# Performance work log

Measured on AMD Instinct MI355X. Metric: run time of the kernel, lower is better.

Reference implementation:

```python
import jax, jax.numpy as jnp
import numpy as np

NUM_CLASSES = 80
SCORE_THR = 0.2
NMS_THR = 0.3
MAX_PER_IMAGE = 100
TOPK_PER_CLASS = 100  # cap on pre-NMS candidates per (image, class); >= max_per_image
ANCHOR_MASK = [[6, 7, 8], [3, 4, 5], [0, 1, 2]]
COCO_ANCHORS = np.array([[10, 13], [16, 30], [33, 23], [30, 61], [62, 45],
                         [59, 119], [116, 90], [156, 198], [373, 326]], dtype=np.float32)


def yolo_head(feats, layer_anchors, num_classes, input_shape):
    # feats: [B, 3*(5+C), gh, gw]
    B = feats.shape[0]
    gh, gw = feats.shape[2], feats.shape[3]
    na = layer_anchors.shape[0]
    f = feats.reshape(B, na, num_classes + 5, gh, gw).transpose(0, 3, 4, 1, 2)  # [B,gh,gw,3,5+C]
    gy, gx = jnp.meshgrid(jnp.arange(gh), jnp.arange(gw), indexing='ij')
    grid = jnp.stack([gx, gy], axis=-1).astype(f.dtype)[None, :, :, None, :]  # [1,gh,gw,1,2]
    # literal translation: divide by tensor([gh, gw]) (square grids in practice)
    box_xy = (jax.nn.sigmoid(f[..., :2]) + grid) / jnp.array([gh, gw], f.dtype)
    box_wh = jnp.exp(f[..., 2:4]) * layer_anchors[None, None, None, :, :] / input_shape[None, None, None, None, :]
    conf = jax.nn.sigmoid(f[..., 4:5])
    probs = jax.nn.sigmoid(f[..., 5:])
    return box_xy, box_wh, conf, probs


def yolo_correct_boxes(box_xy, box_wh, input_shape, image_shape):
    box_yx = box_xy[..., ::-1]
    box_hw = box_wh[..., ::-1]
    new_shape = jnp.round(image_shape * jnp.min(input_shape / image_shape))
    offset = (input_shape - new_shape) / 2.0 / input_shape
    scale = input_shape / new_shape
    box_yx = (box_yx - offset) * scale
    box_hw = box_hw * scale
    mins = box_yx - box_hw / 2.0
    maxes = box_yx + box_hw / 2.0
    boxes = jnp.concatenate([mins, maxes], axis=-1)  # (ymin, xmin, ymax, xmax)
    return boxes * jnp.concatenate([image_shape, image_shape])


def decode_layer(feats, layer_anchors, input_shape, image_shape):
    box_xy, box_wh, conf, probs = yolo_head(feats, layer_anchors, NUM_CLASSES, input_shape)
    boxes = yolo_correct_boxes(box_xy, box_wh, input_shape, image_shape)  # [B,gh,gw,3,4]
    B = feats.shape[0]
    return boxes.reshape(B, -1, 4), (conf * probs).reshape(B, -1, NUM_CLASSES)


def pairwise_iou(b):
    # b: [K,4] (y1,x1,y2,x2)
    y1, x1, y2, x2 = b[:, 0], b[:, 1], b[:, 2], b[:, 3]
    area = jnp.maximum(y2 - y1, 0) * jnp.maximum(x2 - x1, 0)
    iy1 = jnp.maximum(y1[:, None], y1[None, :])
    ix1 = jnp.maximum(x1[:, None], x1[None, :])
    iy2 = jnp.minimum(y2[:, None], y2[None, :])
    ix2 = jnp.minimum(x2[:, None], x2[None, :])
    inter = jnp.maximum(iy2 - iy1, 0) * jnp.maximum(ix2 - ix1, 0)
    return inter / (area[:, None] + area[None, :] - inter + 1e-9)


def greedy_nms(boxes, valid):
    # boxes [K,4] sorted by descending score; valid [K] bool. Returns keep mask [K].
    K = boxes.shape[0]
    iou = jax.lax.stop_gradient(pairwise_iou(boxes))
    idx = jnp.arange(K)
    def body(i, sup):
        keep_i = valid[i] & (~sup[i])
        return sup | (keep_i & (iou[i] > NMS_THR) & (idx > i))
    sup = jax.lax.fori_loop(0, K, body, jnp.zeros((K,), bool))
    return valid & (~sup)


def setup_inputs() -> dict:
    key = jax.random.key(0)
    k0, k1, k2 = jax.random.split(key, 3)
    B, F = 16, 3 * (5 + NUM_CLASSES)
    feat0 = jax.random.normal(k0, (B, F, 19, 19), jnp.float32)
    feat1 = jax.random.normal(k1, (B, F, 38, 38), jnp.float32)
    feat2 = jax.random.normal(k2, (B, F, 76, 76), jnp.float32)
    anchors = jnp.asarray(COCO_ANCHORS)
    image_shape = jnp.array([480.0, 640.0], jnp.float32)
    return {"feat0": feat0, "feat1": feat1, "feat2": feat2,
            "anchors": anchors, "image_shape": image_shape}


def reference(feat0, feat1, feat2, anchors, image_shape):
    input_shape = jnp.array([feat0.shape[2] * 32, feat0.shape[3] * 32], jnp.float32)
    feats = [feat0, feat1, feat2]
    boxes_l, scores_l = [], []
    for l in range(3):
        b, s = decode_layer(feats[l], anchors[np.array(ANCHOR_MASK[l])], input_shape, image_shape)
        boxes_l.append(b)
        scores_l.append(s)
    boxes = jnp.concatenate(boxes_l, axis=1)    # [B,N,4]
    scores = jnp.concatenate(scores_l, axis=1)  # [B,N,C]
    B = scores.shape[0]
    sc = scores.transpose(0, 2, 1)              # [B,C,N]
    top_s, top_i = jax.lax.top_k(sc, TOPK_PER_CLASS)              # [B,C,K]
    top_b = jnp.take_along_axis(boxes[:, None, :, :], top_i[..., None], axis=2)  # [B,C,K,4]
    valid = top_s >= SCORE_THR
    keep = jax.vmap(jax.vmap(greedy_nms))(top_b, valid)           # [B,C,K]
    cand = jnp.where(keep, top_s, -1.0)
    flat_s = cand.reshape(B, -1)                 # [B, C*K]
    flat_b = top_b.reshape(B, -1, 4)
    sel_s, sel_i = jax.lax.top_k(flat_s, MAX_PER_IMAGE)           # [B,100]
    sel_b = jnp.take_along_axis(flat_b, sel_i[..., None], axis=1)  # [B,100,4]
    sel_c = (sel_i // TOPK_PER_CLASS).astype(jnp.float32)
    # dets: (ymin, xmin, ymax, xmax, score, class); score == -1 marks padding
    return jnp.concatenate([sel_b, sel_s[..., None], sel_c[..., None]], axis=-1)
```

## Files before the change

kernel.cpp:

```cpp
#include <hip/hip_runtime.h>
#include <hip/hip_bf16.h>


#define NTOT   22743
#define NCLS   80
#define TOPK   100
#define KPAD   22752
#define NVEC   2842
#define Q_L1   17328
#define Q_L0   21660
#define SCORE_THR 0.2f
#define NMS_THR   0.3f

__device__ __forceinline__ float sig_exact(float x) {
    return 1.0f / (1.0f + expf(-x));
}
__device__ __forceinline__ float sig_fast(float x) {
    return __builtin_amdgcn_rcpf(1.0f + __expf(-x));
}

__global__ __launch_bounds__(256) void k_decode(
    const float* __restrict__ f0, const float* __restrict__ f1,
    const float* __restrict__ f2, const float* __restrict__ anchors,
    const float* __restrict__ imshape, float4* __restrict__ boxes,
    float* __restrict__ conf_q, int total) {
    int gid = blockIdx.x * 256 + threadIdx.x;
    if (gid >= total) return;
    int b = gid / NTOT; int p = gid - b * NTOT;

    const float* f; int ghw, gw, l, off, a, s;
    if (p < 1083)      { f=f0; off=0;    ghw=361;  gw=19; l=0; int r=p;      a=r/361;  s=r-a*361;  }
    else if (p < 5415) { f=f1; off=1083; ghw=1444; gw=38; l=1; int r=p-1083; a=r/1444; s=r-a*1444; }
    else               { f=f2; off=5415; ghw=5776; gw=76; l=2; int r=p-5415; a=r/5776; s=r-a*5776; }
    int y = s / gw, x = s - y * gw;

    const float* q = f + ((size_t)(b * 255 + a * 85) * ghw + s);
    float tx = q[0], ty = q[ghw], tw = q[2*ghw], th = q[3*ghw], tc = q[4*ghw];

    int arow = (2 - l) * 3 + a;
    float aw = anchors[arow * 2], ah = anchors[arow * 2 + 1];
    float imh = imshape[0], imw = imshape[1];
    float gf = (float)gw;

    float bxx = (sig_exact(tx) + (float)x) / gf;
    float bxy = (sig_exact(ty) + (float)y) / gf;
    float bw  = expf(tw) * aw / 608.0f;
    float bh  = expf(th) * ah / 608.0f;

    float r  = fminf(608.0f / imh, 608.0f / imw);
    float nh = rintf(imh * r), nw = rintf(imw * r);
    float offy = (608.0f - nh) / 2.0f / 608.0f;
    float offx = (608.0f - nw) / 2.0f / 608.0f;
    float scy = 608.0f / nh, scx = 608.0f / nw;

    float cy = (bxy - offy) * scy;
    float cx = (bxx - offx) * scx;
    float hh = bh * scy, ww = bw * scx;

    int n = off + 3 * s + a;
    boxes[(size_t)b * NTOT + n] =
        make_float4((cy - hh / 2.0f) * imh, (cx - ww / 2.0f) * imw,
                    (cy + hh / 2.0f) * imh, (cx + ww / 2.0f) * imw);
    int qi = (l == 2) ? (a * 5776 + s)
           : (l == 1) ? (Q_L1 + a * 1444 + s)
                      : (Q_L0 + a * 361 + s);
    conf_q[(size_t)b * KPAD + qi] = sig_exact(tc);
}

#define SEG_A  346560
#define SEG_AB 433200
#define SEG_T  519840
__global__ __launch_bounds__(256) void k_score(
    const float* __restrict__ f0, const float* __restrict__ f1,
    const float* __restrict__ f2, const float* __restrict__ conf_q,
    unsigned short* __restrict__ keybuf, int total) {
    int gid = blockIdx.x * 256 + threadIdx.x;
    if (gid >= total) return;
    const int b = gid / SEG_T;
    const int w = gid - b * SEG_T;

    if (w < SEG_AB) {
        const float* f; int a, c, s, qbase, ghw;
        if (w < SEG_A) {
            a = w / 115520; int r = w - a * 115520;
            c = r / 1444;   s = (r - c * 1444) * 4;
            f = f2; ghw = 5776; qbase = a * 5776;
        } else {
            int t = w - SEG_A;
            a = t / 28880;  int r = t - a * 28880;
            c = r / 361;    s = (r - c * 361) * 4;
            f = f1; ghw = 1444; qbase = Q_L1 + a * 1444;
        }
        const float4 lg = *(const float4*)(f + ((size_t)(b * 255 + a * 85 + 5 + c) * ghw + s));
        const float4 cf = *(const float4*)(conf_q + (size_t)b * KPAD + qbase + s);
        ushort4 k;
        k.x = (unsigned short)(__float_as_uint(cf.x * sig_fast(lg.x)) >> 16);
        k.y = (unsigned short)(__float_as_uint(cf.y * sig_fast(lg.y)) >> 16);
        k.z = (unsigned short)(__float_as_uint(cf.z * sig_fast(lg.z)) >> 16);
        k.w = (unsigned short)(__float_as_uint(cf.w * sig_fast(lg.w)) >> 16);
        *(ushort4*)(keybuf + ((size_t)(b * NCLS + c)) * KPAD + qbase + s) = k;
    } else {
        int t = w - SEG_AB;
        int a = t / 28880;  int r = t - a * 28880;
        int c = r / 361;    int s = r - c * 361;
        int qi = Q_L0 + a * 361 + s;
        float lg = f0[((size_t)(b * 255 + a * 85 + 5 + c) * 361 + s)];
        float cf = conf_q[(size_t)b * KPAD + qi];
        keybuf[((size_t)(b * NCLS + c)) * KPAD + qi] =
            (unsigned short)(__float_as_uint(cf * sig_fast(lg)) >> 16);
    }
}

__device__ void find_pivot(unsigned* hist, int H, unsigned target,
                           unsigned* suf, unsigned* sh_p, unsigned* sh_above) {
    const int tid = threadIdx.x;
    const int per = H >> 8;
    if (tid < 256) {
        unsigned acc = 0;
        for (int u = 0; u < per; ++u) acc += hist[tid * per + u];
        suf[tid] = acc;
    }
    __syncthreads();
    for (int off = 1; off < 256; off <<= 1) {
        unsigned v = 0;
        if (tid < 256) v = (tid + off < 256) ? suf[tid + off] : 0u;
        __syncthreads();
        if (tid < 256) suf[tid] += v;
        __syncthreads();
    }
    if (tid < 256) {
        unsigned mysuf = suf[tid];
        unsigned nxt = (tid == 255) ? 0u : suf[tid + 1];
        if (mysuf >= target && nxt < target) {
            unsigned above = nxt;
            for (int h = tid * per + per - 1; h >= tid * per; --h) {
                unsigned c2 = above + hist[h];
                if (c2 >= target) { *sh_p = (unsigned)h; *sh_above = above; break; }
                above = c2;
            }
        }
    }
    __syncthreads();
}

__device__ __forceinline__ void collect_cand(
    int b, int c, int q, const float* __restrict__ f0,
    const float* __restrict__ f1, const float* __restrict__ f2,
    const float* __restrict__ conf_q, unsigned long long* buf,
    unsigned* sh_cnt) {
    int a, s, nbase, ghw;
    const float* f;
    if (q < Q_L1)      { a = q / 5776;  s = q - a * 5776;  f = f2; ghw = 5776; nbase = 5415; }
    else if (q < Q_L0) { int r = q - Q_L1; a = r / 1444; s = r - a * 1444; f = f1; ghw = 1444; nbase = 1083; }
    else               { int r = q - Q_L0; a = r / 361;  s = r - a * 361;  f = f0; ghw = 361;  nbase = 0;    }
    float t  = f[((size_t)(b * 255 + a * 85 + 5 + c)) * ghw + s];
    float cf = conf_q[(size_t)b * KPAD + q];
    float sce = cf * sig_exact(t);
    int n = nbase + 3 * s + a;
    unsigned slot = atomicAdd(sh_cnt, 1u);
    if (slot < 512)
        buf[slot] = (((unsigned long long)__float_as_uint(sce)) << 32)
                    | (unsigned)(~n);
}

__global__ __launch_bounds__(512, 8) void k_topk(
    const float* __restrict__ f0, const float* __restrict__ f1,
    const float* __restrict__ f2, const float* __restrict__ conf_q,
    const unsigned short* __restrict__ keybuf,
    const float4* __restrict__ boxes, float* __restrict__ top_s,
    float4* __restrict__ top_b) {
    __shared__ unsigned int histp[4096];
    __shared__ unsigned long long buf[512];
    __shared__ unsigned int wsum[4];
    __shared__ unsigned int sh_p, sh_cnt;

    const int tid = threadIdx.x;
    const int row = blockIdx.x;
    const int b = row / NCLS, c = row - b * NCLS;
    const unsigned short* kr = keybuf + (size_t)row * KPAD;
    const uint4* kv = (const uint4*)kr;

    for (int i = tid; i < 4096; i += 512) histp[i] = 0;
    if (tid == 0) sh_cnt = 0;
    __syncthreads();

    uint4 v[6];
    bool  val[6];
    #pragma unroll
    for (int k = 0; k < 6; ++k) {
        int g = tid + k * 512;
        val[k] = (g < NVEC);
        v[k] = val[k] ? kv[g] : make_uint4(0, 0, 0, 0);
    }
    const bool hastail = (tid < NTOT - NVEC * 8);
    unsigned tailk = hastail ? (unsigned)kr[NVEC * 8 + tid] : 0u;

    #pragma unroll
    for (int k = 0; k < 6; ++k) if (val[k]) {
        unsigned ks[8] = { v[k].x & 0xFFFFu, v[k].x >> 16, v[k].y & 0xFFFFu, v[k].y >> 16,
                           v[k].z & 0xFFFFu, v[k].z >> 16, v[k].w & 0xFFFFu, v[k].w >> 16 };
        #pragma unroll
        for (int j = 0; j < 8; ++j)
            atomicAdd(&histp[ks[j] >> 2], 1u << (((ks[j] >> 1) & 1u) * 16));
    }
    if (hastail) atomicAdd(&histp[tailk >> 2], 1u << (((tailk >> 1) & 1u) * 16));
    __syncthreads();

    {
        const int lane = tid & 63;
        unsigned own = 0;
        if (tid < 256) {
            #pragma unroll
            for (int u = 0; u < 16; ++u) {
                unsigned w = histp[tid * 16 + u];
                own += (w & 0xFFFFu) + (w >> 16);
            }
        }
        unsigned acc = own;
        #pragma unroll
        for (int d = 1; d < 64; d <<= 1) {
            unsigned vv = __shfl_down(acc, d, 64);
            if (lane + d < 64) acc += vv;
        }
        if (tid < 256 && lane == 0) wsum[tid >> 6] = acc;
        __syncthreads();
        if (tid < 256) {
            unsigned tail = 0;
            for (int w2 = (tid >> 6) + 1; w2 < 4; ++w2) tail += wsum[w2];
            unsigned suft = acc + tail;
            unsigned nxt  = suft - own;
            if (suft >= TOPK && nxt < TOPK) {
                unsigned above = nxt;
                for (int bb = 31; bb >= 0; --bb) {
                    unsigned w = histp[tid * 16 + (bb >> 1)];
                    unsigned cnt = (bb & 1) ? (w >> 16) : (w & 0xFFFFu);
                    if (above + cnt >= TOPK) { sh_p = (unsigned)(tid * 32 + bb); break; }
                    above += cnt;
                }
            }
        }
        __syncthreads();
    }
    const unsigned kthr = sh_p > 0 ? ((sh_p - 1) << 1) : 0u;

    #pragma unroll
    for (int k = 0; k < 6; ++k) if (val[k]) {
        unsigned ks[8] = { v[k].x & 0xFFFFu, v[k].x >> 16, v[k].y & 0xFFFFu, v[k].y >> 16,
                           v[k].z & 0xFFFFu, v[k].z >> 16, v[k].w & 0xFFFFu, v[k].w >> 16 };
        #pragma unroll
        for (int j = 0; j < 8; ++j)
            if (ks[j] >= kthr)
                collect_cand(b, c, (tid + k * 512) * 8 + j, f0, f1, f2, conf_q, buf, &sh_cnt);
    }
    if (hastail && tailk >= kthr)
        collect_cand(b, c, NVEC * 8 + tid, f0, f1, f2, conf_q, buf, &sh_cnt);
    __syncthreads();

    const int M = (int)min(sh_cnt, 512u);
    if (tid < M) {
        unsigned long long mykey = buf[tid];
        int rank = 0;
        for (int j = 0; j < M; ++j) rank += (buf[j] > mykey);
        if (rank < TOPK) {
            int n = (int)(~(unsigned)mykey);
            top_s[(size_t)row * TOPK + rank] = __uint_as_float((unsigned)(mykey >> 32));
            top_b[(size_t)row * TOPK + rank] = boxes[(size_t)b * NTOT + n];
        }
    }
}

__global__ __launch_bounds__(256) void k_nms(
    const float* __restrict__ top_s, const float4* __restrict__ top_b,
    float* __restrict__ cand) {
    const int lane = threadIdx.x & 63;
    const int row  = blockIdx.x * 4 + (threadIdx.x >> 6);
    const float4* bb = top_b + (size_t)row * TOPK;
    const float*  ss = top_s + (size_t)row * TOPK;

    const int j0 = lane, j1 = lane + 64;
    const bool v1 = (j1 < TOPK);
    float4 B0 = bb[j0];
    float  s0 = ss[j0];
    float4 B1 = v1 ? bb[j1] : make_float4(0.f, 0.f, 0.f, 0.f);
    float  s1 = v1 ? ss[j1] : -1.0f;
    float ar0 = fmaxf(B0.z - B0.x, 0.f) * fmaxf(B0.w - B0.y, 0.f);
    float ar1 = fmaxf(B1.z - B1.x, 0.f) * fmaxf(B1.w - B1.y, 0.f);
    int sup0 = 0, sup1 = 0;

    for (int i = 0; i < TOPK; ++i) {
        const int src = i & 63;
        const bool hi = (i >= 64);
        float yi1 = __shfl(hi ? B1.x : B0.x, src, 64);
        float xi1 = __shfl(hi ? B1.y : B0.y, src, 64);
        float yi2 = __shfl(hi ? B1.z : B0.z, src, 64);
        float xi2 = __shfl(hi ? B1.w : B0.w, src, 64);
        float si  = __shfl(hi ? s1   : s0,   src, 64);
        int  supi = __shfl(hi ? sup1 : sup0, src, 64);
        bool keep_i = (si >= SCORE_THR) && (supi == 0);
        if (keep_i) {
            float ari = fmaxf(yi2 - yi1, 0.f) * fmaxf(xi2 - xi1, 0.f);
            if (j0 > i) {
                float ty1 = fmaxf(yi1, B0.x), tx1 = fmaxf(xi1, B0.y);
                float ty2 = fminf(yi2, B0.z), tx2 = fminf(xi2, B0.w);
                float inter = fmaxf(ty2 - ty1, 0.f) * fmaxf(tx2 - tx1, 0.f);
                float iou = inter / (ari + ar0 - inter + 1e-9f);
                if (iou > NMS_THR) sup0 = 1;
            }
            if (v1 && j1 > i) {
                float ty1 = fmaxf(yi1, B1.x), tx1 = fmaxf(xi1, B1.y);
                float ty2 = fminf(yi2, B1.z), tx2 = fminf(xi2, B1.w);
                float inter = fmaxf(ty2 - ty1, 0.f) * fmaxf(tx2 - tx1, 0.f);
                float iou = inter / (ari + ar1 - inter + 1e-9f);
                if (iou > NMS_THR) sup1 = 1;
            }
        }
    }
    cand[(size_t)row * TOPK + j0] = (s0 >= SCORE_THR && sup0 == 0) ? s0 : -1.0f;
    if (v1)
        cand[(size_t)row * TOPK + j1] = (s1 >= SCORE_THR && sup1 == 0) ? s1 : -1.0f;
}

__global__ __launch_bounds__(256) void k_final(
    const float* __restrict__ cand, const float4* __restrict__ top_b,
    float* __restrict__ out) {
    __shared__ float cs[8000];
    __shared__ unsigned int hist[4096];
    __shared__ unsigned long long buf[512];
    __shared__ unsigned int suf[256];
    __shared__ unsigned int sh_kp, sh_p1, sh_above1, sh_p2, sh_above2, sh_cnt;

    const int tid = threadIdx.x, b = blockIdx.x;
    if (tid == 0) { sh_kp = 0; sh_cnt = 0; }
    for (int i = tid; i < 4096; i += 256) hist[i] = 0;
    __syncthreads();

    unsigned lk = 0;
    for (int i = tid; i < 8000; i += 256) {
        float v = cand[b * 8000 + i];
        cs[i] = v;
        if (v > -0.5f) lk++;
    }
    atomicAdd(&sh_kp, lk);
    __syncthreads();
    unsigned Kp = sh_kp;

    if (Kp >= TOPK) {
        for (int i = tid; i < 8000; i += 256)
            if (cs[i] > -0.5f) atomicAdd(&hist[__float_as_uint(cs[i]) >> 19], 1u);
        __syncthreads();
        find_pivot(hist, 2048, TOPK, suf, &sh_p1, &sh_above1);
        unsigned p1 = sh_p1, above1 = sh_above1;
        for (int i = tid; i < 4096; i += 256) hist[i] = 0;
        __syncthreads();
        for (int i = tid; i < 8000; i += 256) {
            float v = cs[i];
            if (v > -0.5f) {
                unsigned bits = __float_as_uint(v);
                if ((bits >> 19) == p1) atomicAdd(&hist[(bits >> 7) & 0xFFFu], 1u);
            }
        }
        __syncthreads();
        find_pivot(hist, 4096, TOPK - above1, suf, &sh_p2, &sh_above2);
        unsigned p2 = sh_p2;
        for (int i = tid; i < 8000; i += 256) {
            float v = cs[i];
            if (v > -0.5f) {
                unsigned bits = __float_as_uint(v);
                unsigned b1 = bits >> 19;
                if (b1 > p1 || (b1 == p1 && ((bits >> 7) & 0xFFFu) >= p2)) {
                    unsigned slot = atomicAdd(&sh_cnt, 1u);
                    if (slot < 512)
                        buf[slot] = (((unsigned long long)bits) << 32) | (unsigned)(~i);
                }
            }
        }
    } else {
        for (int i = tid; i < 8000; i += 256) {
            float v = cs[i];
            if (v > -0.5f) {
                unsigned slot = atomicAdd(&sh_cnt, 1u);
                buf[slot] = (((unsigned long long)__float_as_uint(v)) << 32) | (unsigned)(~i);
            }
        }
        __syncthreads();
        if (tid == 0) {
            unsigned need = TOPK - Kp, got = 0;
            for (int i = 0; i < 8000 && got < need; ++i)
                if (cs[i] <= -0.5f) { buf[Kp + got] = (unsigned)(~i); got++; }
        }
    }
    __syncthreads();

    const int M2 = (Kp >= TOPK) ? (int)min(sh_cnt, 512u) : (int)TOPK;
    for (int i = tid; i < M2; i += 256) {
        unsigned long long key = buf[i];
        int rank = 0;
        for (int j = 0; j < M2; ++j) rank += (buf[j] > key);
        if (rank < TOPK) {
            int fi = (int)(~(unsigned)key);
            int c = fi / TOPK; int kk = fi - c * TOPK;
            float4 bb = top_b[((size_t)b * NCLS + c) * TOPK + kk];
            int base = (b * TOPK + rank) * 6;
            out[base + 0] = bb.x; out[base + 1] = bb.y;
            out[base + 2] = bb.z; out[base + 3] = bb.w;
            out[base + 4] = cs[fi]; out[base + 5] = (float)c;
        }
    }
}

extern "C" void kernel_launch(void* const* d_in, const int* in_sizes, int n_in,
                              void* d_out, int out_size, void* d_ws, size_t ws_size,
                              hipStream_t stream) {
    (void)n_in; (void)out_size; (void)ws_size;
    const float* f0      = (const float*)d_in[0];
    const float* f1      = (const float*)d_in[1];
    const float* f2      = (const float*)d_in[2];
    const float* anchors = (const float*)d_in[3];
    const float* imshape = (const float*)d_in[4];
    const int B = in_sizes[0] / (255 * 19 * 19);

    char* ws = (char*)d_ws;
    size_t o = 0;
    unsigned short* keybuf = (unsigned short*)(ws + o);
    o += (size_t)B * NCLS * KPAD * sizeof(unsigned short);
    float4* boxes  = (float4*)(ws + o); o += (size_t)B * NTOT * sizeof(float4);
    float*  conf_q = (float*)(ws + o);  o += (size_t)B * KPAD * sizeof(float);
    float*  top_s  = (float*)(ws + o);  o += (size_t)B * NCLS * TOPK * sizeof(float);
    float4* top_b  = (float4*)(ws + o); o += (size_t)B * NCLS * TOPK * sizeof(float4);
    float*  cand   = (float*)(ws + o);  o += (size_t)B * NCLS * TOPK * sizeof(float);
    float*  out    = (float*)d_out;

    const int total = B * NTOT;
    k_decode<<<(total + 255) / 256, 256, 0, stream>>>(f0, f1, f2, anchors, imshape,
                                                      boxes, conf_q, total);
    const int stotal = B * SEG_T;
    k_score<<<(stotal + 255) / 256, 256, 0, stream>>>(f0, f1, f2, conf_q,
                                                      keybuf, stotal);
    k_topk<<<B * NCLS, 512, 0, stream>>>(f0, f1, f2, conf_q, keybuf, boxes,
                                         top_s, top_b);
    k_nms<<<(B * NCLS) / 4, 256, 0, stream>>>(top_s, top_b, cand);
    k_final<<<B, 256, 0, stream>>>(cand, top_b, out);
}
```

Measured before the change: 266.7 us.

## Fuse class-score computation into top-k kernel, drop keybuf round trip

Removes the separate k_score kernel that wrote 16-bit score keys for every (image, class, anchor) to a global key buffer. k_topk now reads the class logits and confidences directly, computes the keys in registers, and builds its histogram from them, keeping the keys in registers for the candidate-collection pass. This eliminates one kernel launch and the write and reread of the key buffer. In exchange k_topk carries more registers per thread and more arithmetic, and its input reads are spread across three feature maps.

```diff
diff --git a/kernel.cpp b/kernel.cpp
--- a/kernel.cpp
+++ b/kernel.cpp
@@ -6,9 +6,9 @@
 #define NCLS   80
 #define TOPK   100
 #define KPAD   22752
-#define NVEC   2842
 #define Q_L1   17328
 #define Q_L0   21660
+#define NVQ    5415
 #define SCORE_THR 0.2f
 #define NMS_THR   0.3f
 
@@ -65,82 +65,6 @@
            : (l == 1) ? (Q_L1 + a * 1444 + s)
                       : (Q_L0 + a * 361 + s);
     conf_q[(size_t)b * KPAD + qi] = sig_exact(tc);
-}
-
-#define SEG_A  346560
-#define SEG_AB 433200
-#define SEG_T  519840
-__global__ __launch_bounds__(256) void k_score(
-    const float* __restrict__ f0, const float* __restrict__ f1,
-    const float* __restrict__ f2, const float* __restrict__ conf_q,
-    unsigned short* __restrict__ keybuf, int total) {
-    int gid = blockIdx.x * 256 + threadIdx.x;
-    if (gid >= total) return;
-    const int b = gid / SEG_T;
-    const int w = gid - b * SEG_T;
-
-    if (w < SEG_AB) {
-        const float* f; int a, c, s, qbase, ghw;
-        if (w < SEG_A) {
-            a = w / 115520; int r = w - a * 115520;
-            c = r / 1444;   s = (r - c * 1444) * 4;
-            f = f2; ghw = 5776; qbase = a * 5776;
-        } else {
-            int t = w - SEG_A;
-            a = t / 28880;  int r = t - a * 28880;
-            c = r / 361;    s = (r - c * 361) * 4;
-            f = f1; ghw = 1444; qbase = Q_L1 + a * 1444;
-        }
-        const float4 lg = *(const float4*)(f + ((size_t)(b * 255 + a * 85 + 5 + c) * ghw + s));
-        const float4 cf = *(const float4*)(conf_q + (size_t)b * KPAD + qbase + s);
-        ushort4 k;
-        k.x = (unsigned short)(__float_as_uint(cf.x * sig_fast(lg.x)) >> 16);
-        k.y = (unsigned short)(__float_as_uint(cf.y * sig_fast(lg.y)) >> 16);
-        k.z = (unsigned short)(__float_as_uint(cf.z * sig_fast(lg.z)) >> 16);
-        k.w = (unsigned short)(__float_as_uint(cf.w * sig_fast(lg.w)) >> 16);
-        *(ushort4*)(keybuf + ((size_t)(b * NCLS + c)) * KPAD + qbase + s) = k;
-    } else {
-        int t = w - SEG_AB;
-        int a = t / 28880;  int r = t - a * 28880;
-        int c = r / 361;    int s = r - c * 361;
-        int qi = Q_L0 + a * 361 + s;
-        float lg = f0[((size_t)(b * 255 + a * 85 + 5 + c) * 361 + s)];
-        float cf = conf_q[(size_t)b * KPAD + qi];
-        keybuf[((size_t)(b * NCLS + c)) * KPAD + qi] =
-            (unsigned short)(__float_as_uint(cf * sig_fast(lg)) >> 16);
-    }
-}
-
-__device__ void find_pivot(unsigned* hist, int H, unsigned target,
-                           unsigned* suf, unsigned* sh_p, unsigned* sh_above) {
-    const int tid = threadIdx.x;
-    const int per = H >> 8;
-    if (tid < 256) {
-        unsigned acc = 0;
-        for (int u = 0; u < per; ++u) acc += hist[tid * per + u];
-        suf[tid] = acc;
-    }
-    __syncthreads();
-    for (int off = 1; off < 256; off <<= 1) {
-        unsigned v = 0;
-        if (tid < 256) v = (tid + off < 256) ? suf[tid + off] : 0u;
-        __syncthreads();
-        if (tid < 256) suf[tid] += v;
-        __syncthreads();
-    }
-    if (tid < 256) {
-        unsigned mysuf = suf[tid];
-        unsigned nxt = (tid == 255) ? 0u : suf[tid + 1];
-        if (mysuf >= target && nxt < target) {
-            unsigned above = nxt;
-            for (int h = tid * per + per - 1; h >= tid * per; --h) {
-                unsigned c2 = above + hist[h];
-                if (c2 >= target) { *sh_p = (unsigned)h; *sh_above = above; break; }
-                above = c2;
-            }
-        }
-    }
-    __syncthreads();
 }
 
 __device__ __forceinline__ void collect_cand(
@@ -166,7 +90,6 @@
 __global__ __launch_bounds__(512, 8) void k_topk(
     const float* __restrict__ f0, const float* __restrict__ f1,
     const float* __restrict__ f2, const float* __restrict__ conf_q,
-    const unsigned short* __restrict__ keybuf,
     const float4* __restrict__ boxes, float* __restrict__ top_s,
     float4* __restrict__ top_b) {
     __shared__ unsigned int histp[4096];
@@ -177,33 +100,53 @@
     const int tid = threadIdx.x;
     const int row = blockIdx.x;
     const int b = row / NCLS, c = row - b * NCLS;
-    const unsigned short* kr = keybuf + (size_t)row * KPAD;
-    const uint4* kv = (const uint4*)kr;
+    const float* cfrow = conf_q + (size_t)b * KPAD;
 
     for (int i = tid; i < 4096; i += 512) histp[i] = 0;
     if (tid == 0) sh_cnt = 0;
     __syncthreads();
 
-    uint4 v[6];
-    bool  val[6];
+    uint2 kreg[11];
     #pragma unroll
-    for (int k = 0; k < 6; ++k) {
-        int g = tid + k * 512;
-        val[k] = (g < NVEC);
-        v[k] = val[k] ? kv[g] : make_uint4(0, 0, 0, 0);
-    }
-    const bool hastail = (tid < NTOT - NVEC * 8);
-    unsigned tailk = hastail ? (unsigned)kr[NVEC * 8 + tid] : 0u;
-
+    for (int k = 0; k < 11; ++k) {
+        const int g = tid + k * 512;
+        const bool valid = (k < 10) || (g < NVQ);
+        kreg[k] = make_uint2(0u, 0u);
+        if (valid) {
+            const int q = g * 4;
+            const float* lp; int s;
+            if (q < Q_L1) { int a = q / 5776; s = q - a * 5776;
+                lp = f2 + (size_t)(b * 255 + a * 85 + 5 + c) * 5776; }
+            else          { int r = q - Q_L1; int a = r / 1444; s = r - a * 1444;
+                lp = f1 + (size_t)(b * 255 + a * 85 + 5 + c) * 1444; }
+            const float4 lg = *(const float4*)(lp + s);
+            const float4 cf = *(const float4*)(cfrow + q);
+            unsigned kx = __float_as_uint(cf.x * sig_fast(lg.x)) >> 16;
+            unsigned ky = __float_as_uint(cf.y * sig_fast(lg.y)) >> 16;
+            unsigned kz = __float_as_uint(cf.z * sig_fast(lg.z)) >> 16;
+            unsigned kw = __float_as_uint(cf.w * sig_fast(lg.w)) >> 16;
+            kreg[k] = make_uint2(kx | (ky << 16), kz | (kw << 16));
+            atomicAdd(&histp[kx >> 2], 1u << (((kx >> 1) & 1u) * 16));
+            atomicAdd(&histp[ky >> 2], 1u << (((ky >> 1) & 1u) * 16));
+            atomicAdd(&histp[kz >> 2], 1u << (((kz >> 1) & 1u) * 16));
+            atomicAdd(&histp[kw >> 2], 1u << (((kw >> 1) & 1u) * 16));
+        }
+    }
+    unsigned k0[3];
     #pragma unroll
-    for (int k = 0; k < 6; ++k) if (val[k]) {
-        unsigned ks[8] = { v[k].x & 0xFFFFu, v[k].x >> 16, v[k].y & 0xFFFFu, v[k].y >> 16,
-                           v[k].z & 0xFFFFu, v[k].z >> 16, v[k].w & 0xFFFFu, v[k].w >> 16 };
-        #pragma unroll
-        for (int j = 0; j < 8; ++j)
-            atomicAdd(&histp[ks[j] >> 2], 1u << (((ks[j] >> 1) & 1u) * 16));
-    }
-    if (hastail) atomicAdd(&histp[tailk >> 2], 1u << (((tailk >> 1) & 1u) * 16));
+    for (int it = 0; it < 3; ++it) {
+        const int idx = tid + it * 512;
+        const bool valid = (idx < NTOT - Q_L0);
+        k0[it] = 0u;
+        if (valid) {
+            const int a = idx / 361, s = idx - a * 361;
+            float lg = f0[(size_t)(b * 255 + a * 85 + 5 + c) * 361 + s];
+            float cf = cfrow[Q_L0 + idx];
+            unsigned kk = __float_as_uint(cf * sig_fast(lg)) >> 16;
+            k0[it] = kk;
+            atomicAdd(&histp[kk >> 2], 1u << (((kk >> 1) & 1u) * 16));
+        }
+    }
     __syncthreads();
 
     {
@@ -244,16 +187,24 @@
     const unsigned kthr = sh_p > 0 ? ((sh_p - 1) << 1) : 0u;
 
     #pragma unroll
-    for (int k = 0; k < 6; ++k) if (val[k]) {
-        unsigned ks[8] = { v[k].x & 0xFFFFu, v[k].x >> 16, v[k].y & 0xFFFFu, v[k].y >> 16,
-                           v[k].z & 0xFFFFu, v[k].z >> 16, v[k].w & 0xFFFFu, v[k].w >> 16 };
-        #pragma unroll
-        for (int j = 0; j < 8; ++j)
-            if (ks[j] >= kthr)
-                collect_cand(b, c, (tid + k * 512) * 8 + j, f0, f1, f2, conf_q, buf, &sh_cnt);
-    }
-    if (hastail && tailk >= kthr)
-        collect_cand(b, c, NVEC * 8 + tid, f0, f1, f2, conf_q, buf, &sh_cnt);
+    for (int k = 0; k < 11; ++k) {
+        const int g = tid + k * 512;
+        if ((k < 10) || (g < NVQ)) {
+            const int q = g * 4;
+            unsigned ks[4] = { kreg[k].x & 0xFFFFu, kreg[k].x >> 16,
+                               kreg[k].y & 0xFFFFu, kreg[k].y >> 16 };
+            #pragma unroll
+            for (int j = 0; j < 4; ++j)
+                if (ks[j] >= kthr)
+                    collect_cand(b, c, q + j, f0, f1, f2, conf_q, buf, &sh_cnt);
+        }
+    }
+    #pragma unroll
+    for (int it = 0; it < 3; ++it) {
+        const int idx = tid + it * 512;
+        if (idx < NTOT - Q_L0 && k0[it] >= kthr)
+            collect_cand(b, c, Q_L0 + idx, f0, f1, f2, conf_q, buf, &sh_cnt);
+    }
     __syncthreads();
 
     const int M = (int)min(sh_cnt, 512u);
@@ -320,6 +271,38 @@
         cand[(size_t)row * TOPK + j1] = (s1 >= SCORE_THR && sup1 == 0) ? s1 : -1.0f;
 }
 
+__device__ void find_pivot(unsigned* hist, int H, unsigned target,
+                           unsigned* suf, unsigned* sh_p, unsigned* sh_above) {
+    const int tid = threadIdx.x;
+    const int per = H >> 8;
+    if (tid < 256) {
+        unsigned acc = 0;
+        for (int u = 0; u < per; ++u) acc += hist[tid * per + u];
+        suf[tid] = acc;
+    }
+    __syncthreads();
+    for (int off = 1; off < 256; off <<= 1) {
+        unsigned v = 0;
+        if (tid < 256) v = (tid + off < 256) ? suf[tid + off] : 0u;
+        __syncthreads();
+        if (tid < 256) suf[tid] += v;
+        __syncthreads();
+    }
+    if (tid < 256) {
+        unsigned mysuf = suf[tid];
+        unsigned nxt = (tid == 255) ? 0u : suf[tid + 1];
+        if (mysuf >= target && nxt < target) {
+            unsigned above = nxt;
+            for (int h = tid * per + per - 1; h >= tid * per; --h) {
+                unsigned c2 = above + hist[h];
+                if (c2 >= target) { *sh_p = (unsigned)h; *sh_above = above; break; }
+                above = c2;
+            }
+        }
+    }
+    __syncthreads();
+}
+
 __global__ __launch_bounds__(256) void k_final(
     const float* __restrict__ cand, const float4* __restrict__ top_b,
     float* __restrict__ out) {
@@ -421,8 +404,6 @@
 
     char* ws = (char*)d_ws;
     size_t o = 0;
-    unsigned short* keybuf = (unsigned short*)(ws + o);
-    o += (size_t)B * NCLS * KPAD * sizeof(unsigned short);
     float4* boxes  = (float4*)(ws + o); o += (size_t)B * NTOT * sizeof(float4);
     float*  conf_q = (float*)(ws + o);  o += (size_t)B * KPAD * sizeof(float);
     float*  top_s  = (float*)(ws + o);  o += (size_t)B * NCLS * TOPK * sizeof(float);
@@ -433,10 +414,7 @@
     const int total = B * NTOT;
     k_decode<<<(total + 255) / 256, 256, 0, stream>>>(f0, f1, f2, anchors, imshape,
                                                       boxes, conf_q, total);
-    const int stotal = B * SEG_T;
-    k_score<<<(stotal + 255) / 256, 256, 0, stream>>>(f0, f1, f2, conf_q,
-                                                      keybuf, stotal);
-    k_topk<<<B * NCLS, 512, 0, stream>>>(f0, f1, f2, conf_q, keybuf, boxes,
+    k_topk<<<B * NCLS, 512, 0, stream>>>(f0, f1, f2, conf_q, boxes,
                                          top_s, top_b);
     k_nms<<<(B * NCLS) / 4, 256, 0, stream>>>(top_s, top_b, cand);
     k_final<<<B, 256, 0, stream>>>(cand, top_b, out);
```

Result: slower. 328.9 us (+23.3%).
